# Optimization experiments

Hardware: AMD Instinct MI355X
Metric: run time of the kernel (lower is better)

Reference implementation:

```python
import jax, jax.numpy as jnp
import numpy as np

N, E, B = 100000, 1600000, 128
F_E, F_X, F_U, H = 128, 128, 128, 64
F_U_OUT = 128


def setup_inputs() -> dict:
    key = jax.random.key(0)
    ks = jax.random.split(key, 16)
    s = lambda fan_in: 1.0 / np.sqrt(fan_in)
    inp = {
        "x": jax.random.normal(ks[0], (N, F_X), jnp.float32),
        "e": jax.random.normal(ks[1], (E, F_E), jnp.float32),
        "u": jax.random.normal(ks[2], (B, F_U), jnp.float32),
        "edge_index": jax.random.randint(ks[3], (2, E), 0, N, jnp.int64),
        "batch": jnp.sort(jax.random.randint(ks[4], (N,), 0, B, jnp.int64)),
        # attention projection params
        "Wk_e": jax.random.uniform(ks[5], (F_E, H), jnp.float32, -s(F_E), s(F_E)),
        "bk_e": jnp.zeros((H,), jnp.float32),
        "Wq_e": jax.random.uniform(ks[6], (F_U, H), jnp.float32, -s(F_U), s(F_U)),
        "bq_e": jnp.zeros((H,), jnp.float32),
        "Wk_x": jax.random.uniform(ks[7], (F_X, H), jnp.float32, -s(F_X), s(F_X)),
        "bk_x": jnp.zeros((H,), jnp.float32),
        "Wq_x": jax.random.uniform(ks[8], (F_U, H), jnp.float32, -s(F_U), s(F_U)),
        "bq_x": jnp.zeros((H,), jnp.float32),
        # phi_u (model_fn = single Linear)
        "Wu": jax.random.uniform(ks[9], (F_E + F_X + F_U, F_U_OUT), jnp.float32,
                                  -s(F_E + F_X + F_U), s(F_E + F_X + F_U)),
        "bu": jnp.zeros((F_U_OUT,), jnp.float32),
    }
    return inp


def reference(x, e, u, edge_index, batch,
              Wk_e, bk_e, Wq_e, bq_e, Wk_x, bk_x, Wq_x, bq_x, Wu, bu):
    num_graphs = u.shape[0]
    src = edge_index[0]
    e_batch = batch[src]                       # [E] graph id per edge

    # edge attention: sigmoid(<k_e, q_e>) per edge, then scatter-add per graph
    k = e @ Wk_e + bk_e                        # [E, H]
    q = (u @ Wq_e + bq_e)[e_batch]             # [E, H] gather
    a_e = jax.nn.sigmoid(jnp.sum(k * q, axis=-1, keepdims=True))  # [E, 1]
    e_agg = jax.ops.segment_sum(a_e * e, e_batch, num_segments=num_graphs)  # [B, F_E]

    # node attention
    kx = x @ Wk_x + bk_x                       # [N, H]
    qx = (u @ Wq_x + bq_x)[batch]              # [N, H] gather
    a_x = jax.nn.sigmoid(jnp.sum(kx * qx, axis=-1, keepdims=True))  # [N, 1]
    x_agg = jax.ops.segment_sum(a_x * x, batch, num_segments=num_graphs)  # [B, F_X]

    out = jnp.concatenate([x_agg, e_agg, u], axis=1)  # [B, F_X+F_E+F_U]
    return out @ Wu + bu                        # [B, F_U_OUT]
```

## Files before the change

kernel.cpp:

```cpp
#include <hip/hip_runtime.h>
#include <hip/hip_bf16.h>


#define FDIM 128
#define BGRAPH 128
#define HDIM 64
#define SLICES 16
#define CAP 16384
#define CURSOR_STRIDE 16
#define SC_THREADS 512
#define SC_ITEMS 16

typedef float vf4 __attribute__((ext_vector_type(4)));

__device__ inline vf4 ldnt4(const float* p) {
    return __builtin_nontemporal_load(reinterpret_cast<const vf4*>(p));
}

__global__ __launch_bounds__(SC_THREADS) void prep_kernel(
    const int* __restrict__ src, const int* __restrict__ batch,
    int* __restrict__ cursor,
    int* __restrict__ order,
    float* __restrict__ e_agg,
    float* __restrict__ x_agg,
    const float* __restrict__ x,
    const float* __restrict__ u,
    const float* __restrict__ Wk_e, const float* __restrict__ bk_e,
    const float* __restrict__ Wq_e, const float* __restrict__ bq_e,
    const float* __restrict__ Wk_x, const float* __restrict__ bk_x,
    const float* __restrict__ Wq_x, const float* __restrict__ bq_x,
    float* __restrict__ v_e, float* __restrict__ c_e,
    int E, int N, int nb_edge)
{
    const int t = threadIdx.x;

    if (blockIdx.x < nb_edge) {
        __shared__ int lh[BGRAPH];
        __shared__ int s_base[BGRAPH];
        if (t < BGRAPH) lh[t] = 0;
        __syncthreads();

        const int base0 = blockIdx.x * SC_THREADS * SC_ITEMS;
        int gv[SC_ITEMS], rv[SC_ITEMS];
#pragma unroll
        for (int k = 0; k < SC_ITEMS; ++k) {
            const int i = base0 + k * SC_THREADS + t;
            if (i < E) {
                const int g = batch[__builtin_nontemporal_load(src + i)];
                gv[k] = g;
                rv[k] = atomicAdd(&lh[g], 1);
            } else {
                gv[k] = -1; rv[k] = 0;
            }
        }
        __syncthreads();
        if (t < BGRAPH) {
            const int n = lh[t];
            const int b = (n > 0) ? atomicAdd(&cursor[t * CURSOR_STRIDE], n) : 0;
            s_base[t] = t * CAP + b;
        }
        __syncthreads();
#pragma unroll
        for (int k = 0; k < SC_ITEMS; ++k) {
            const int i = base0 + k * SC_THREADS + t;
            if (gv[k] >= 0) order[s_base[gv[k]] + rv[k]] = i;
        }
    } else {
        const int g = blockIdx.x - nb_edge;
        __shared__ float su[FDIM];
        __shared__ float sqe[HDIM];
        __shared__ float sqx[HDIM];
        __shared__ float s_vx[FDIM];
        __shared__ float s_cx;

        if (t < FDIM) {
            e_agg[g * FDIM + t] = 0.f;
            su[t] = u[g * FDIM + t];
        }
        __syncthreads();

        if (t < HDIM) {
            float acc = bq_e[t];
            for (int f = 0; f < FDIM; ++f) acc += su[f] * Wq_e[f * HDIM + t];
            sqe[t] = acc;
        } else if (t < 2 * HDIM) {
            const int h = t - HDIM;
            float acc = bq_x[h];
            for (int f = 0; f < FDIM; ++f) acc += su[f] * Wq_x[f * HDIM + h];
            sqx[h] = acc;
        }
        __syncthreads();

        if (t < FDIM) {
            float acce = 0.f, accx = 0.f;
            for (int h = 0; h < HDIM; ++h) {
                acce += Wk_e[t * HDIM + h] * sqe[h];
                accx += Wk_x[t * HDIM + h] * sqx[h];
            }
            v_e[g * FDIM + t] = acce;
            s_vx[t] = accx;
        }
        if (t == 0) {
            float ce = 0.f, cx = 0.f;
            for (int h = 0; h < HDIM; ++h) { ce += bk_e[h] * sqe[h]; cx += bk_x[h] * sqx[h]; }
            c_e[g] = ce;
            s_cx = cx;
        }
        __syncthreads();

        int lo = 0, hi = N;
        while (lo < hi) { int mid = (lo + hi) >> 1; if (batch[mid] < g) lo = mid + 1; else hi = mid; }
        const int start = lo;
        hi = N;
        while (lo < hi) { int mid = (lo + hi) >> 1; if (batch[mid] < g + 1) lo = mid + 1; else hi = mid; }
        const int end = lo;

        const int hidx = t >> 5;
        const int hl   = t & 31;
        const vf4 fv = *reinterpret_cast<const vf4*>(&s_vx[4 * hl]);
        const float cg = s_cx;

        vf4 acc = (vf4)(0.f);
        for (int row = start + hidx; row < end; row += 16) {
            const vf4 fe = ldnt4(x + (size_t)row * FDIM + 4 * hl);
            float d = fe.x * fv.x + fe.y * fv.y + fe.z * fv.z + fe.w * fv.w;
            d += __shfl_xor(d, 1);
            d += __shfl_xor(d, 2);
            d += __shfl_xor(d, 4);
            d += __shfl_xor(d, 8);
            d += __shfl_xor(d, 16);
            const float a = 1.f / (1.f + __expf(-(d + cg)));
            acc.x += a * fe.x; acc.y += a * fe.y; acc.z += a * fe.z; acc.w += a * fe.w;
        }

        __shared__ float s_red[16][FDIM];
        s_red[hidx][4 * hl + 0] = acc.x;
        s_red[hidx][4 * hl + 1] = acc.y;
        s_red[hidx][4 * hl + 2] = acc.z;
        s_red[hidx][4 * hl + 3] = acc.w;
        __syncthreads();

        if (t < FDIM) {
            float ssum = 0.f;
#pragma unroll
            for (int k = 0; k < 16; ++k) ssum += s_red[k][t];
            x_agg[g * FDIM + t] = ssum;
        }
    }
}

__global__ __launch_bounds__(1024, 8) void agg_kernel(
    const float* __restrict__ e,
    const int*   __restrict__ order,
    const int*   __restrict__ cursor,
    const float* __restrict__ v_e, const float* __restrict__ c_e,
    float* __restrict__ e_agg)
{
    const int tid  = threadIdx.x;
    const int hidx = tid >> 5;
    const int hl   = tid & 31;
    __shared__ float s_red[32][FDIM];

    const int g = blockIdx.x / SLICES;
    const int s = blockIdx.x % SLICES;
    const int len = cursor[g * CURSOR_STRIDE];
    const int lo = g * CAP;
    const int chunk = (len + SLICES - 1) / SLICES;
    const int clo = lo + s * chunk;
    const int chi = min(clo + chunk, lo + len);

    const vf4 fv = *reinterpret_cast<const vf4*>(v_e + g * FDIM + 4 * hl);
    const float cg = c_e[g];

    vf4 acc = (vf4)(0.f);

    int pos = clo + hidx;
    int j1 = 0, j2 = 0;
    vf4 fe0 = (vf4)(0.f), fe1 = (vf4)(0.f);
    if (pos < chi) {
        const int j0 = order[pos];
        fe0 = ldnt4(e + (size_t)j0 * FDIM + 4 * hl);
    }
    if (pos + 32 < chi) {
        j1 = order[pos + 32];
        fe1 = ldnt4(e + (size_t)j1 * FDIM + 4 * hl);
    }
    if (pos + 64 < chi) j2 = order[pos + 64];

    for (; pos < chi; pos += 32) {
        const int j3 = (pos + 96 < chi) ? order[pos + 96] : 0;
        vf4 fe2 = (vf4)(0.f);
        if (pos + 64 < chi)
            fe2 = ldnt4(e + (size_t)j2 * FDIM + 4 * hl);

        float d = fe0.x * fv.x + fe0.y * fv.y + fe0.z * fv.z + fe0.w * fv.w;
        d += __shfl_xor(d, 1);
        d += __shfl_xor(d, 2);
        d += __shfl_xor(d, 4);
        d += __shfl_xor(d, 8);
        d += __shfl_xor(d, 16);
        const float a = 1.f / (1.f + __expf(-(d + cg)));
        acc.x += a * fe0.x; acc.y += a * fe0.y; acc.z += a * fe0.z; acc.w += a * fe0.w;

        fe0 = fe1; fe1 = fe2; j2 = j3;
    }

    s_red[hidx][4 * hl + 0] = acc.x;
    s_red[hidx][4 * hl + 1] = acc.y;
    s_red[hidx][4 * hl + 2] = acc.z;
    s_red[hidx][4 * hl + 3] = acc.w;
    __syncthreads();

    if (tid < FDIM) {
        float ssum = 0.f;
#pragma unroll
        for (int k = 0; k < 32; ++k) ssum += s_red[k][tid];
        unsafeAtomicAdd(&e_agg[g * FDIM + tid], ssum);
    }
}

__global__ __launch_bounds__(128) void final_kernel(
    const float* __restrict__ x_agg, const float* __restrict__ e_agg,
    const float* __restrict__ u,
    const float* __restrict__ Wu, const float* __restrict__ bu,
    float* __restrict__ out)
{
    const int g = blockIdx.x;
    const int o = threadIdx.x;
    __shared__ float cat[3 * FDIM];
    cat[o]            = x_agg[g * FDIM + o];
    cat[FDIM + o]     = e_agg[g * FDIM + o];
    cat[2 * FDIM + o] = u[g * FDIM + o];
    __syncthreads();

    float acc = bu[o];
#pragma unroll 8
    for (int r = 0; r < 3 * FDIM; ++r) acc += cat[r] * Wu[r * FDIM + o];
    out[g * FDIM + o] = acc;
}

extern "C" void kernel_launch(void* const* d_in, const int* in_sizes, int n_in,
                              void* d_out, int out_size, void* d_ws, size_t ws_size,
                              hipStream_t stream) {
    const float* x          = (const float*)d_in[0];
    const float* e          = (const float*)d_in[1];
    const float* u          = (const float*)d_in[2];
    const int*   edge_index = (const int*)d_in[3];
    const int*   batch      = (const int*)d_in[4];
    const float* Wk_e = (const float*)d_in[5];
    const float* bk_e = (const float*)d_in[6];
    const float* Wq_e = (const float*)d_in[7];
    const float* bq_e = (const float*)d_in[8];
    const float* Wk_x = (const float*)d_in[9];
    const float* bk_x = (const float*)d_in[10];
    const float* Wq_x = (const float*)d_in[11];
    const float* bq_x = (const float*)d_in[12];
    const float* Wu   = (const float*)d_in[13];
    const float* bu   = (const float*)d_in[14];

    const int N = in_sizes[4];
    const int E = in_sizes[3] / 2;
    const int* src = edge_index;

    float* ws    = (float*)d_ws;
    float* v_e   = ws;
    float* c_e   = v_e + BGRAPH * FDIM;
    float* e_agg = c_e + BGRAPH;
    float* x_agg = e_agg + BGRAPH * FDIM;
    int*   cursor = (int*)(x_agg + BGRAPH * FDIM);
    int*   order  = cursor + BGRAPH * CURSOR_STRIDE;

    hipMemsetAsync(cursor, 0, BGRAPH * CURSOR_STRIDE * sizeof(int), stream);

    const int nb_edge = (E + SC_THREADS * SC_ITEMS - 1) / (SC_THREADS * SC_ITEMS);
    prep_kernel<<<nb_edge + BGRAPH, SC_THREADS, 0, stream>>>(
        src, batch, cursor, order, e_agg, x_agg, x,
        u, Wk_e, bk_e, Wq_e, bq_e, Wk_x, bk_x, Wq_x, bq_x,
        v_e, c_e, E, N, nb_edge);

    agg_kernel<<<BGRAPH * SLICES, 1024, 0, stream>>>(
        e, order, cursor, v_e, c_e, e_agg);

    final_kernel<<<BGRAPH, 128, 0, stream>>>(
        x_agg, e_agg, u, Wu, bu, (float*)d_out);
}
```

Baseline: 213.1 us.

## Split node aggregation across two blocks per graph and stage edge ids in LDS

Node-attention work per graph is now split across two blocks that interleave rows, prefetch the next row and combine results with atomic adds. The zeroing of x_agg, e_agg and the cursors is folded into one memset. In the edge aggregation kernel, each slice's order indices are first copied into shared memory so the prefetch loop reads ids from LDS instead of chasing global memory. The aim is better parallelism and shorter dependency chains, at the cost of extra atomics, a redundant q projection per block pair, and a 4K-int shared buffer that could limit occupancy.

Result: faster. 202.8 us (-4.8%).

```diff
diff --git a/kernel.cpp b/kernel.cpp
--- a/kernel.cpp
+++ b/kernel.cpp
@@ -10,6 +10,7 @@
 #define CURSOR_STRIDE 16
 #define SC_THREADS 512
 #define SC_ITEMS 16
+#define MAXCHUNK (CAP / SLICES)
 
 typedef float vf4 __attribute__((ext_vector_type(4)));
 
@@ -21,7 +22,6 @@
     const int* __restrict__ src, const int* __restrict__ batch,
     int* __restrict__ cursor,
     int* __restrict__ order,
-    float* __restrict__ e_agg,
     float* __restrict__ x_agg,
     const float* __restrict__ x,
     const float* __restrict__ u,
@@ -66,17 +66,16 @@
             if (gv[k] >= 0) order[s_base[gv[k]] + rv[k]] = i;
         }
     } else {
-        const int g = blockIdx.x - nb_edge;
+        const int g2  = blockIdx.x - nb_edge;
+        const int g   = g2 >> 1;
+        const int par = g2 & 1;
         __shared__ float su[FDIM];
         __shared__ float sqe[HDIM];
         __shared__ float sqx[HDIM];
         __shared__ float s_vx[FDIM];
         __shared__ float s_cx;
 
-        if (t < FDIM) {
-            e_agg[g * FDIM + t] = 0.f;
-            su[t] = u[g * FDIM + t];
-        }
+        if (t < FDIM) su[t] = u[g * FDIM + t];
         __syncthreads();
 
         if (t < HDIM) {
@@ -97,14 +96,18 @@
                 acce += Wk_e[t * HDIM + h] * sqe[h];
                 accx += Wk_x[t * HDIM + h] * sqx[h];
             }
-            v_e[g * FDIM + t] = acce;
+            if (par == 0) v_e[g * FDIM + t] = acce;
             s_vx[t] = accx;
         }
         if (t == 0) {
-            float ce = 0.f, cx = 0.f;
-            for (int h = 0; h < HDIM; ++h) { ce += bk_e[h] * sqe[h]; cx += bk_x[h] * sqx[h]; }
-            c_e[g] = ce;
+            float cx = 0.f;
+            for (int h = 0; h < HDIM; ++h) cx += bk_x[h] * sqx[h];
             s_cx = cx;
+            if (par == 0) {
+                float ce = 0.f;
+                for (int h = 0; h < HDIM; ++h) ce += bk_e[h] * sqe[h];
+                c_e[g] = ce;
+            }
         }
         __syncthreads();
 
@@ -121,8 +124,12 @@
         const float cg = s_cx;
 
         vf4 acc = (vf4)(0.f);
-        for (int row = start + hidx; row < end; row += 16) {
-            const vf4 fe = ldnt4(x + (size_t)row * FDIM + 4 * hl);
+        int row = start + 2 * hidx + par;
+        vf4 fe = (vf4)(0.f);
+        if (row < end) fe = ldnt4(x + (size_t)row * FDIM + 4 * hl);
+        for (; row < end; row += 32) {
+            vf4 fen = (vf4)(0.f);
+            if (row + 32 < end) fen = ldnt4(x + (size_t)(row + 32) * FDIM + 4 * hl);
             float d = fe.x * fv.x + fe.y * fv.y + fe.z * fv.z + fe.w * fv.w;
             d += __shfl_xor(d, 1);
             d += __shfl_xor(d, 2);
@@ -131,6 +138,7 @@
             d += __shfl_xor(d, 16);
             const float a = 1.f / (1.f + __expf(-(d + cg)));
             acc.x += a * fe.x; acc.y += a * fe.y; acc.z += a * fe.z; acc.w += a * fe.w;
+            fe = fen;
         }
 
         __shared__ float s_red[16][FDIM];
@@ -144,7 +152,7 @@
             float ssum = 0.f;
 #pragma unroll
             for (int k = 0; k < 16; ++k) ssum += s_red[k][t];
-            x_agg[g * FDIM + t] = ssum;
+            unsafeAtomicAdd(&x_agg[g * FDIM + t], ssum);
         }
     }
 }
@@ -160,49 +168,43 @@
     const int hidx = tid >> 5;
     const int hl   = tid & 31;
     __shared__ float s_red[32][FDIM];
+    __shared__ int s_ids[MAXCHUNK];
 
     const int g = blockIdx.x / SLICES;
     const int s = blockIdx.x % SLICES;
     const int len = cursor[g * CURSOR_STRIDE];
-    const int lo = g * CAP;
     const int chunk = (len + SLICES - 1) / SLICES;
-    const int clo = lo + s * chunk;
-    const int chi = min(clo + chunk, lo + len);
+    const int clo = s * chunk;
+    const int cnt = min(chunk, len - clo);
+
+    for (int i = tid; i < cnt; i += 1024) s_ids[i] = order[g * CAP + clo + i];
+    __syncthreads();
 
     const vf4 fv = *reinterpret_cast<const vf4*>(v_e + g * FDIM + 4 * hl);
     const float cg = c_e[g];
 
     vf4 acc = (vf4)(0.f);
 
-    int pos = clo + hidx;
-    int j1 = 0, j2 = 0;
-    vf4 fe0 = (vf4)(0.f), fe1 = (vf4)(0.f);
-    if (pos < chi) {
-        const int j0 = order[pos];
-        fe0 = ldnt4(e + (size_t)j0 * FDIM + 4 * hl);
-    }
-    if (pos + 32 < chi) {
-        j1 = order[pos + 32];
-        fe1 = ldnt4(e + (size_t)j1 * FDIM + 4 * hl);
-    }
-    if (pos + 64 < chi) j2 = order[pos + 64];
-
-    for (; pos < chi; pos += 32) {
-        const int j3 = (pos + 96 < chi) ? order[pos + 96] : 0;
-        vf4 fe2 = (vf4)(0.f);
-        if (pos + 64 < chi)
-            fe2 = ldnt4(e + (size_t)j2 * FDIM + 4 * hl);
-
-        float d = fe0.x * fv.x + fe0.y * fv.y + fe0.z * fv.z + fe0.w * fv.w;
+    int p = hidx;
+    vf4 f0 = (vf4)(0.f), f1 = (vf4)(0.f), f2 = (vf4)(0.f);
+    if (p < cnt)      f0 = ldnt4(e + (size_t)s_ids[p]      * FDIM + 4 * hl);
+    if (p + 32 < cnt) f1 = ldnt4(e + (size_t)s_ids[p + 32] * FDIM + 4 * hl);
+    if (p + 64 < cnt) f2 = ldnt4(e + (size_t)s_ids[p + 64] * FDIM + 4 * hl);
+
+    for (; p < cnt; p += 32) {
+        vf4 f3 = (vf4)(0.f);
+        if (p + 96 < cnt) f3 = ldnt4(e + (size_t)s_ids[p + 96] * FDIM + 4 * hl);
+
+        float d = f0.x * fv.x + f0.y * fv.y + f0.z * fv.z + f0.w * fv.w;
         d += __shfl_xor(d, 1);
         d += __shfl_xor(d, 2);
         d += __shfl_xor(d, 4);
         d += __shfl_xor(d, 8);
         d += __shfl_xor(d, 16);
         const float a = 1.f / (1.f + __expf(-(d + cg)));
-        acc.x += a * fe0.x; acc.y += a * fe0.y; acc.z += a * fe0.z; acc.w += a * fe0.w;
-
-        fe0 = fe1; fe1 = fe2; j2 = j3;
+        acc.x += a * f0.x; acc.y += a * f0.y; acc.z += a * f0.z; acc.w += a * f0.w;
+
+        f0 = f1; f1 = f2; f2 = f3;
     }
 
     s_red[hidx][4 * hl + 0] = acc.x;
@@ -270,11 +272,12 @@
     int*   cursor = (int*)(x_agg + BGRAPH * FDIM);
     int*   order  = cursor + BGRAPH * CURSOR_STRIDE;
 
-    hipMemsetAsync(cursor, 0, BGRAPH * CURSOR_STRIDE * sizeof(int), stream);
+    hipMemsetAsync(e_agg, 0,
+        (2 * BGRAPH * FDIM + BGRAPH * CURSOR_STRIDE) * sizeof(float), stream);
 
     const int nb_edge = (E + SC_THREADS * SC_ITEMS - 1) / (SC_THREADS * SC_ITEMS);
-    prep_kernel<<<nb_edge + BGRAPH, SC_THREADS, 0, stream>>>(
-        src, batch, cursor, order, e_agg, x_agg, x,
+    prep_kernel<<<nb_edge + 2 * BGRAPH, SC_THREADS, 0, stream>>>(
+        src, batch, cursor, order, x_agg, x,
         u, Wk_e, bk_e, Wq_e, bq_e, Wk_x, bk_x, Wq_x, bq_x,
         v_e, c_e, E, N, nb_edge);
 
```
